# Optimization experiments

Hardware: AMD Instinct MI355X
Metric: run time of the kernel (lower is better)

## Reference

```python
import jax, jax.numpy as jnp
import numpy as np

B, L, DK, DV, H, DKL, DVL, R = 64, 4096, 128, 128, 4, 64, 128, 128


def setup_inputs() -> dict:
    key = jax.random.key(0)
    ks = jax.random.split(key, 7)
    K = jax.random.normal(ks[0], (B, L, DK), dtype=jnp.float32)
    V = jax.random.normal(ks[1], (B, L, DV), dtype=jnp.float32)
    mask = jax.random.uniform(ks[2], (B, L)) < 0.25
    mask = mask.at[:, 0].set(False)
    # Learned parameters (Wq is zeros at init in the original; use small random
    # values so the softmax is non-degenerate for correctness testing)
    Wq = jax.random.normal(ks[3], (H, DKL), dtype=jnp.float32) * 0.02
    Wk = jax.random.normal(ks[4], (DK, H, DKL), dtype=jnp.float32) / np.sqrt(DK)
    Wv = jax.random.normal(ks[5], (DV, H, DVL), dtype=jnp.float32) / np.sqrt(DV)
    Wo = jax.random.normal(ks[6], (H, DVL, R), dtype=jnp.float32) / np.sqrt(H * DVL)
    return {"K": K, "V": V, "mask": mask, "Wq": Wq, "Wk": Wk, "Wv": Wv, "Wo": Wo}


def reference(K, V, mask, Wq, Wk, Wv, Wo):
    # scale = 1/sqrt(dim_q), dim_q == dim_k
    scale = 1.0 / jnp.sqrt(jnp.asarray(K.shape[-1], K.dtype))
    Kp = jnp.einsum('bld,dhk->blhk', K, Wk)          # (B, L, H, DKL)
    Vp = jnp.einsum('ble,ehv->blhv', V, Wv)          # (B, L, H, DVL)
    QK = jnp.einsum('hk,blhk->blh', Wq, Kp)          # (B, L, H)
    QK = jnp.where(mask[..., None], -jnp.inf, QK)    # mask over set axis L
    w = jax.nn.softmax(scale * QK, axis=-2)          # softmax over L (dim=-2)
    # nanmean over the set axis (masked positions contribute w=0; NaN entries,
    # if present in V, are skipped exactly as torch.nanmean does)
    QKV = jnp.nanmean(w[..., None] * Vp, axis=-3)    # (B, H, DVL)
    return jnp.einsum('bhv,hvr->br', QKV, Wo)        # (B, R)
```

## Files before the change

kernel.cpp:

```cpp
#include <hip/hip_runtime.h>
#include <math.h>

#define BB   64
#define LL   4096
#define DKC  128
#define DVC  128
#define HC   4
#define DKLC 64
#define DVLC 128
#define RC   128

#define NCA  64
#define CA   64
#define NCB  16
#define CB   256
#define SUB  4

typedef float f4v __attribute__((ext_vector_type(4)));
__device__ __forceinline__ float4 ntload4(const float4* p) {
    f4v v = __builtin_nontemporal_load((const f4v*)p);
    return make_float4(v.x, v.y, v.z, v.w);
}

__global__ __launch_bounds__(512) void k_foldq(const float* __restrict__ Wq,
                                               const float* __restrict__ Wk,
                                               float* __restrict__ q) {
    int t = threadIdx.x;
    int h = t >> 7;
    int d = t & 127;
    float acc = 0.f;
#pragma unroll 8
    for (int k = 0; k < DKLC; ++k)
        acc += Wq[h * DKLC + k] * Wk[(d * HC + h) * DKLC + k];
    q[h * DKC + d] = acc;
}

__global__ __launch_bounds__(256) void k_score(const float* __restrict__ K,
                                               const int*   __restrict__ mask,
                                               const float* __restrict__ q,
                                               float* __restrict__ P4,
                                               float* __restrict__ stats) {
    const int bid = blockIdx.x;
    const int b   = bid >> 6;
    const int sp  = bid & (NCA - 1);
    const int l0  = sp * CA;
    const int t   = threadIdx.x;
    const int rg  = t >> 5;
    const int i4  = t & 31;

    __shared__ float4 part[CA][33];
    __shared__ float  redm[4][HC];
    __shared__ float  redz[4][HC];

    float4 qf[HC];
#pragma unroll
    for (int h = 0; h < HC; ++h)
        qf[h] = ((const float4*)q)[h * 32 + i4];

    const float4* Kg = (const float4*)(K + ((long)b * LL + l0) * DKC);

#pragma unroll
    for (int it = 0; it < CA / 8; ++it) {
        int r = it * 8 + rg;
        float4 kv = ntload4(&Kg[r * 32 + i4]);
        float4 d;
        d.x = kv.x*qf[0].x + kv.y*qf[0].y + kv.z*qf[0].z + kv.w*qf[0].w;
        d.y = kv.x*qf[1].x + kv.y*qf[1].y + kv.z*qf[1].z + kv.w*qf[1].w;
        d.z = kv.x*qf[2].x + kv.y*qf[2].y + kv.z*qf[2].z + kv.w*qf[2].w;
        d.w = kv.x*qf[3].x + kv.y*qf[3].y + kv.z*qf[3].z + kv.w*qf[3].w;
        part[r][i4] = d;
    }
    __syncthreads();

    const int r2 = t >> 2;
    const int h2 = t & 3;
    float s = 0.f;
#pragma unroll
    for (int c = 0; c < 32; ++c)
        s += ((const float*)part)[(r2 * 33 + c) * 4 + h2];

    int mk = __builtin_nontemporal_load(mask + (long)b * LL + l0 + r2);
    const float scale = 0.08838834764831844f;
    s = mk ? -INFINITY : s * scale;

    float m = s;
#pragma unroll
    for (int off = 4; off <= 32; off <<= 1)
        m = fmaxf(m, __shfl_xor(m, off));
    if ((t & 63) < 4) redm[t >> 6][h2] = m;
    __syncthreads();
    float mm = fmaxf(fmaxf(redm[0][h2], redm[1][h2]),
                     fmaxf(redm[2][h2], redm[3][h2]));
    float mu = (mm == -INFINITY) ? 0.f : mm;

    float p = expf(s - mu);
    float z = p;
#pragma unroll
    for (int off = 4; off <= 32; off <<= 1)
        z += __shfl_xor(z, off);
    if ((t & 63) < 4) redz[t >> 6][h2] = z;
    if (t < HC) stats[(long)bid * 8 + t] = mm;
    __syncthreads();
    if (t < HC)
        stats[(long)bid * 8 + 4 + t] =
            redz[0][t] + redz[1][t] + redz[2][t] + redz[3][t];

    P4[((long)b * LL + l0) * 4 + t] = p;
}

__global__ __launch_bounds__(256) void k_wv(const float* __restrict__ V,
                                            const float* __restrict__ P4,
                                            const float* __restrict__ stats,
                                            float* __restrict__ partWV) {
    const int bid = blockIdx.x;
    const int b   = bid >> 4;
    const int spB = bid & (NCB - 1);
    const int l0  = spB * CB;
    const int t   = threadIdx.x;
    const int rg  = t >> 5;
    const int i4  = t & 31;
    const int w   = t >> 6;

    __shared__ float4 red[4][32][HC];

    float ma[SUB][HC];
#pragma unroll
    for (int j = 0; j < SUB; ++j)
#pragma unroll
        for (int h = 0; h < HC; ++h)
            ma[j][h] = stats[((long)b * NCA + spB * SUB + j) * 8 + h];
    float4 f4[SUB];
#pragma unroll
    for (int h = 0; h < HC; ++h) {
        float m4 = fmaxf(fmaxf(ma[0][h], ma[1][h]), fmaxf(ma[2][h], ma[3][h]));
        float mu4 = (m4 == -INFINITY) ? 0.f : m4;
#pragma unroll
        for (int j = 0; j < SUB; ++j) {
            float f = (ma[j][h] == -INFINITY) ? 0.f : expf(ma[j][h] - mu4);
            ((float*)&f4[j])[h] = f;
        }
    }

    float4 acc[HC];
#pragma unroll
    for (int h = 0; h < HC; ++h) acc[h] = make_float4(0.f, 0.f, 0.f, 0.f);

    const float4* Vb = (const float4*)(V + ((long)b * LL + l0) * DVC);
    const float4* Pb = (const float4*)P4 + (long)b * LL + l0;

#pragma unroll
    for (int j = 0; j < SUB; ++j) {
        float4 fj = f4[j];
#pragma unroll 8
        for (int it = 0; it < 8; ++it) {
            int r = j * 64 + it * 8 + rg;
            float4 w4 = Pb[r];
            float4 vv = ntload4(&Vb[r * 32 + i4]);
            float w0 = w4.x * fj.x, w1 = w4.y * fj.y;
            float w2 = w4.z * fj.z, w3 = w4.w * fj.w;
            acc[0].x += w0*vv.x; acc[0].y += w0*vv.y; acc[0].z += w0*vv.z; acc[0].w += w0*vv.w;
            acc[1].x += w1*vv.x; acc[1].y += w1*vv.y; acc[1].z += w1*vv.z; acc[1].w += w1*vv.w;
            acc[2].x += w2*vv.x; acc[2].y += w2*vv.y; acc[2].z += w2*vv.z; acc[2].w += w2*vv.w;
            acc[3].x += w3*vv.x; acc[3].y += w3*vv.y; acc[3].z += w3*vv.z; acc[3].w += w3*vv.w;
        }
    }

#pragma unroll
    for (int h = 0; h < HC; ++h) {
        acc[h].x += __shfl_xor(acc[h].x, 32);
        acc[h].y += __shfl_xor(acc[h].y, 32);
        acc[h].z += __shfl_xor(acc[h].z, 32);
        acc[h].w += __shfl_xor(acc[h].w, 32);
    }
    if ((t & 63) < 32) {
#pragma unroll
        for (int h = 0; h < HC; ++h) red[w][i4][h] = acc[h];
    }
    __syncthreads();
    if (t < 128) {
        int h = t >> 5, c = t & 31;
        float4 s0 = red[0][c][h], s1 = red[1][c][h];
        float4 s2 = red[2][c][h], s3 = red[3][c][h];
        float4 o;
        o.x = s0.x + s1.x + s2.x + s3.x;
        o.y = s0.y + s1.y + s2.y + s3.y;
        o.z = s0.z + s1.z + s2.z + s3.z;
        o.w = s0.w + s1.w + s2.w + s3.w;
        ((float4*)partWV)[((long)bid * HC + h) * (DVC / 4) + c] = o;
    }
}

__global__ __launch_bounds__(256) void k_out(const float* __restrict__ stats,
                                             const float* __restrict__ partWV,
                                             const float* __restrict__ Wv,
                                             const float* __restrict__ Wo,
                                             float* __restrict__ out) {
    int b = blockIdx.x;
    int t = threadIdx.x;
    __shared__ float WV[HC][DVC];
    __shared__ float QKV[HC * DVLC];
    __shared__ float sc[NCB][HC];
    __shared__ float zinv[HC];

    {
        int h2 = t >> 6, a = t & 63;
        float ma = stats[((long)b * NCA + a) * 8 + h2];
        float za = stats[((long)b * NCA + a) * 8 + 4 + h2];
        float m = ma;
#pragma unroll
        for (int off = 32; off; off >>= 1) m = fmaxf(m, __shfl_xor(m, off));
        float f  = (ma == -INFINITY) ? 0.f : expf(ma - m);
        float fz = f * za;
#pragma unroll
        for (int off = 32; off; off >>= 1) fz += __shfl_xor(fz, off);
        float m4 = ma;
        m4 = fmaxf(m4, __shfl_xor(m4, 1));
        m4 = fmaxf(m4, __shfl_xor(m4, 2));
        if ((a & 3) == 0) sc[a >> 2][h2] = (m4 == -INFINITY) ? 0.f : expf(m4 - m);
        if (a == 0) zinv[h2] = 1.0f / fz;
    }
    __syncthreads();

    for (int j = t; j < HC * DVC; j += 256) {
        int h = j >> 7, e = j & 127;
        float a = 0.f;
#pragma unroll 8
        for (int p = 0; p < NCB; ++p)
            a += sc[p][h] * partWV[(((long)b * NCB + p) * HC + h) * DVC + e];
        WV[h][e] = a * zinv[h];
    }
    __syncthreads();

    for (int j = t; j < HC * DVLC; j += 256) {
        int h = j >> 7, vv = j & 127;
        float a = 0.f;
#pragma unroll 8
        for (int e = 0; e < DVC; ++e)
            a += WV[h][e] * Wv[(e * HC + h) * DVLC + vv];
        QKV[j] = a * (1.0f / LL);
    }
    __syncthreads();

    for (int r = t; r < RC; r += 256) {
        float a = 0.f;
#pragma unroll 8
        for (int i = 0; i < HC * DVLC; ++i)
            a += QKV[i] * Wo[i * RC + r];
        out[b * RC + r] = a;
    }
}

extern "C" void kernel_launch(void* const* d_in, const int* in_sizes, int n_in,
                              void* d_out, int out_size, void* d_ws, size_t ws_size,
                              hipStream_t stream) {
    (void)in_sizes; (void)n_in; (void)out_size; (void)ws_size;
    const float* K    = (const float*)d_in[0];
    const float* V    = (const float*)d_in[1];
    const int*   mask = (const int*)  d_in[2];
    const float* Wq   = (const float*)d_in[3];
    const float* Wk   = (const float*)d_in[4];
    const float* Wv   = (const float*)d_in[5];
    const float* Wo   = (const float*)d_in[6];
    float* out = (float*)d_out;

    float* q      = (float*)d_ws;
    float* stats  = q + 512;
    float* partWV = stats + (long)BB * NCA * 8;
    float* P4     = partWV + (long)BB * NCB * HC * DVC;

    k_foldq<<<1, 512, 0, stream>>>(Wq, Wk, q);
    k_score<<<BB * NCA, 256, 0, stream>>>(K, mask, q, P4, stats);
    k_wv<<<BB * NCB, 256, 0, stream>>>(V, P4, stats, partWV);
    k_out<<<BB, 256, 0, stream>>>(stats, partWV, Wv, Wo, out);
}
```

Measured before the change: 79.89 us.

## Fuse score and weighted-V passes into one kernel per 64-row chunk

Merges the score/softmax-stat kernel and the weighted-V accumulation kernel into a single kernel, so each 64-row chunk computes its probabilities into shared memory and immediately uses them against V. This drops the global P4 round trip and one kernel launch. It also restructures the K dot product so each thread handles two float4s. In exchange, partWV becomes four times larger (64 chunks instead of 16), which enlarges the partial-sum reduction in the output kernel. Shared memory is reused for the final reduction.

```diff
diff --git a/kernel.cpp b/kernel.cpp
--- a/kernel.cpp
+++ b/kernel.cpp
@@ -12,9 +12,6 @@
 
 #define NCA  64
 #define CA   64
-#define NCB  16
-#define CB   256
-#define SUB  4
 
 typedef float f4v __attribute__((ext_vector_type(4)));
 __device__ __forceinline__ float4 ntload4(const float4* p) {
@@ -35,136 +32,106 @@
     q[h * DKC + d] = acc;
 }
 
-__global__ __launch_bounds__(256) void k_score(const float* __restrict__ K,
+__global__ __launch_bounds__(256) void k_fused(const float* __restrict__ K,
+                                               const float* __restrict__ V,
                                                const int*   __restrict__ mask,
                                                const float* __restrict__ q,
-                                               float* __restrict__ P4,
-                                               float* __restrict__ stats) {
+                                               float* __restrict__ stats,
+                                               float* __restrict__ partWV) {
     const int bid = blockIdx.x;
     const int b   = bid >> 6;
-    const int sp  = bid & (NCA - 1);
-    const int l0  = sp * CA;
+    const int a   = bid & (NCA - 1);
+    const int l0  = a * CA;
     const int t   = threadIdx.x;
-    const int rg  = t >> 5;
-    const int i4  = t & 31;
-
-    __shared__ float4 part[CA][33];
+
+    __shared__ float4 partS[CA][17];
+    __shared__ float  P4s[CA * HC];
     __shared__ float  redm[4][HC];
     __shared__ float  redz[4][HC];
 
-    float4 qf[HC];
-#pragma unroll
-    for (int h = 0; h < HC; ++h)
-        qf[h] = ((const float4*)q)[h * 32 + i4];
-
-    const float4* Kg = (const float4*)(K + ((long)b * LL + l0) * DKC);
-
-#pragma unroll
-    for (int it = 0; it < CA / 8; ++it) {
-        int r = it * 8 + rg;
-        float4 kv = ntload4(&Kg[r * 32 + i4]);
-        float4 d;
-        d.x = kv.x*qf[0].x + kv.y*qf[0].y + kv.z*qf[0].z + kv.w*qf[0].w;
-        d.y = kv.x*qf[1].x + kv.y*qf[1].y + kv.z*qf[1].z + kv.w*qf[1].w;
-        d.z = kv.x*qf[2].x + kv.y*qf[2].y + kv.z*qf[2].z + kv.w*qf[2].w;
-        d.w = kv.x*qf[3].x + kv.y*qf[3].y + kv.z*qf[3].z + kv.w*qf[3].w;
-        part[r][i4] = d;
-    }
-    __syncthreads();
-
-    const int r2 = t >> 2;
-    const int h2 = t & 3;
-    float s = 0.f;
-#pragma unroll
-    for (int c = 0; c < 32; ++c)
-        s += ((const float*)part)[(r2 * 33 + c) * 4 + h2];
-
-    int mk = __builtin_nontemporal_load(mask + (long)b * LL + l0 + r2);
-    const float scale = 0.08838834764831844f;
-    s = mk ? -INFINITY : s * scale;
-
-    float m = s;
-#pragma unroll
-    for (int off = 4; off <= 32; off <<= 1)
-        m = fmaxf(m, __shfl_xor(m, off));
-    if ((t & 63) < 4) redm[t >> 6][h2] = m;
-    __syncthreads();
-    float mm = fmaxf(fmaxf(redm[0][h2], redm[1][h2]),
-                     fmaxf(redm[2][h2], redm[3][h2]));
-    float mu = (mm == -INFINITY) ? 0.f : mm;
-
-    float p = expf(s - mu);
-    float z = p;
-#pragma unroll
-    for (int off = 4; off <= 32; off <<= 1)
-        z += __shfl_xor(z, off);
-    if ((t & 63) < 4) redz[t >> 6][h2] = z;
-    if (t < HC) stats[(long)bid * 8 + t] = mm;
-    __syncthreads();
-    if (t < HC)
-        stats[(long)bid * 8 + 4 + t] =
-            redz[0][t] + redz[1][t] + redz[2][t] + redz[3][t];
-
-    P4[((long)b * LL + l0) * 4 + t] = p;
-}
-
-__global__ __launch_bounds__(256) void k_wv(const float* __restrict__ V,
-                                            const float* __restrict__ P4,
-                                            const float* __restrict__ stats,
-                                            float* __restrict__ partWV) {
-    const int bid = blockIdx.x;
-    const int b   = bid >> 4;
-    const int spB = bid & (NCB - 1);
-    const int l0  = spB * CB;
-    const int t   = threadIdx.x;
-    const int rg  = t >> 5;
+    {
+        const int rg = t >> 4;
+        const int i8 = t & 15;
+        float4 qf1[HC], qf2[HC];
+#pragma unroll
+        for (int h = 0; h < HC; ++h) {
+            qf1[h] = ((const float4*)q)[h * 32 + i8];
+            qf2[h] = ((const float4*)q)[h * 32 + i8 + 16];
+        }
+        const float4* Kg = (const float4*)(K + ((long)b * LL + l0) * DKC);
+#pragma unroll
+        for (int it = 0; it < CA / 16; ++it) {
+            int r = it * 16 + rg;
+            float4 k1 = ntload4(&Kg[r * 32 + i8]);
+            float4 k2 = ntload4(&Kg[r * 32 + i8 + 16]);
+            float4 d;
+            d.x = k1.x*qf1[0].x + k1.y*qf1[0].y + k1.z*qf1[0].z + k1.w*qf1[0].w
+                + k2.x*qf2[0].x + k2.y*qf2[0].y + k2.z*qf2[0].z + k2.w*qf2[0].w;
+            d.y = k1.x*qf1[1].x + k1.y*qf1[1].y + k1.z*qf1[1].z + k1.w*qf1[1].w
+                + k2.x*qf2[1].x + k2.y*qf2[1].y + k2.z*qf2[1].z + k2.w*qf2[1].w;
+            d.z = k1.x*qf1[2].x + k1.y*qf1[2].y + k1.z*qf1[2].z + k1.w*qf1[2].w
+                + k2.x*qf2[2].x + k2.y*qf2[2].y + k2.z*qf2[2].z + k2.w*qf2[2].w;
+            d.w = k1.x*qf1[3].x + k1.y*qf1[3].y + k1.z*qf1[3].z + k1.w*qf1[3].w
+                + k2.x*qf2[3].x + k2.y*qf2[3].y + k2.z*qf2[3].z + k2.w*qf2[3].w;
+            partS[r][i8] = d;
+        }
+    }
+    __syncthreads();
+
+    {
+        const int r2 = t >> 2;
+        const int h2 = t & 3;
+        float s = 0.f;
+#pragma unroll
+        for (int c = 0; c < 16; ++c)
+            s += ((const float*)partS)[(r2 * 17 + c) * 4 + h2];
+
+        int mk = __builtin_nontemporal_load(mask + (long)b * LL + l0 + r2);
+        const float scale = 0.08838834764831844f;
+        s = mk ? -INFINITY : s * scale;
+
+        float m = s;
+#pragma unroll
+        for (int off = 4; off <= 32; off <<= 1)
+            m = fmaxf(m, __shfl_xor(m, off));
+        if ((t & 63) < 4) redm[t >> 6][h2] = m;
+        __syncthreads();
+        float mm = fmaxf(fmaxf(redm[0][h2], redm[1][h2]),
+                         fmaxf(redm[2][h2], redm[3][h2]));
+        float mu = (mm == -INFINITY) ? 0.f : mm;
+
+        float p = expf(s - mu);
+        float z = p;
+#pragma unroll
+        for (int off = 4; off <= 32; off <<= 1)
+            z += __shfl_xor(z, off);
+        if ((t & 63) < 4) redz[t >> 6][h2] = z;
+        P4s[t] = p;
+        if (t < HC) stats[(long)bid * 8 + t] = mm;
+        __syncthreads();
+        if (t < HC)
+            stats[(long)bid * 8 + 4 + t] =
+                redz[0][t] + redz[1][t] + redz[2][t] + redz[3][t];
+    }
+
+    const int rg3 = t >> 5;
     const int i4  = t & 31;
     const int w   = t >> 6;
-
-    __shared__ float4 red[4][32][HC];
-
-    float ma[SUB][HC];
-#pragma unroll
-    for (int j = 0; j < SUB; ++j)
-#pragma unroll
-        for (int h = 0; h < HC; ++h)
-            ma[j][h] = stats[((long)b * NCA + spB * SUB + j) * 8 + h];
-    float4 f4[SUB];
-#pragma unroll
-    for (int h = 0; h < HC; ++h) {
-        float m4 = fmaxf(fmaxf(ma[0][h], ma[1][h]), fmaxf(ma[2][h], ma[3][h]));
-        float mu4 = (m4 == -INFINITY) ? 0.f : m4;
-#pragma unroll
-        for (int j = 0; j < SUB; ++j) {
-            float f = (ma[j][h] == -INFINITY) ? 0.f : expf(ma[j][h] - mu4);
-            ((float*)&f4[j])[h] = f;
-        }
-    }
-
     float4 acc[HC];
 #pragma unroll
     for (int h = 0; h < HC; ++h) acc[h] = make_float4(0.f, 0.f, 0.f, 0.f);
 
     const float4* Vb = (const float4*)(V + ((long)b * LL + l0) * DVC);
-    const float4* Pb = (const float4*)P4 + (long)b * LL + l0;
-
-#pragma unroll
-    for (int j = 0; j < SUB; ++j) {
-        float4 fj = f4[j];
-#pragma unroll 8
-        for (int it = 0; it < 8; ++it) {
-            int r = j * 64 + it * 8 + rg;
-            float4 w4 = Pb[r];
-            float4 vv = ntload4(&Vb[r * 32 + i4]);
-            float w0 = w4.x * fj.x, w1 = w4.y * fj.y;
-            float w2 = w4.z * fj.z, w3 = w4.w * fj.w;
-            acc[0].x += w0*vv.x; acc[0].y += w0*vv.y; acc[0].z += w0*vv.z; acc[0].w += w0*vv.w;
-            acc[1].x += w1*vv.x; acc[1].y += w1*vv.y; acc[1].z += w1*vv.z; acc[1].w += w1*vv.w;
-            acc[2].x += w2*vv.x; acc[2].y += w2*vv.y; acc[2].z += w2*vv.z; acc[2].w += w2*vv.w;
-            acc[3].x += w3*vv.x; acc[3].y += w3*vv.y; acc[3].z += w3*vv.z; acc[3].w += w3*vv.w;
-        }
-    }
-
+#pragma unroll
+    for (int it = 0; it < CA / 8; ++it) {
+        int r = it * 8 + rg3;
+        float4 vv = ntload4(&Vb[r * 32 + i4]);
+        float4 w4 = ((const float4*)P4s)[r];
+        acc[0].x += w4.x*vv.x; acc[0].y += w4.x*vv.y; acc[0].z += w4.x*vv.z; acc[0].w += w4.x*vv.w;
+        acc[1].x += w4.y*vv.x; acc[1].y += w4.y*vv.y; acc[1].z += w4.y*vv.z; acc[1].w += w4.y*vv.w;
+        acc[2].x += w4.z*vv.x; acc[2].y += w4.z*vv.y; acc[2].z += w4.z*vv.z; acc[2].w += w4.z*vv.w;
+        acc[3].x += w4.w*vv.x; acc[3].y += w4.w*vv.y; acc[3].z += w4.w*vv.z; acc[3].w += w4.w*vv.w;
+    }
 #pragma unroll
     for (int h = 0; h < HC; ++h) {
         acc[h].x += __shfl_xor(acc[h].x, 32);
@@ -172,6 +139,8 @@
         acc[h].z += __shfl_xor(acc[h].z, 32);
         acc[h].w += __shfl_xor(acc[h].w, 32);
     }
+    float4 (*red)[32][HC] = (float4 (*)[32][HC])partS;
+    __syncthreads();
     if ((t & 63) < 32) {
 #pragma unroll
         for (int h = 0; h < HC; ++h) red[w][i4][h] = acc[h];
@@ -199,7 +168,7 @@
     int t = threadIdx.x;
     __shared__ float WV[HC][DVC];
     __shared__ float QKV[HC * DVLC];
-    __shared__ float sc[NCB][HC];
+    __shared__ float sc[NCA][HC];
     __shared__ float zinv[HC];
 
     {
@@ -210,43 +179,40 @@
 #pragma unroll
         for (int off = 32; off; off >>= 1) m = fmaxf(m, __shfl_xor(m, off));
         float f  = (ma == -INFINITY) ? 0.f : expf(ma - m);
+        sc[a][h2] = f;
         float fz = f * za;
 #pragma unroll
         for (int off = 32; off; off >>= 1) fz += __shfl_xor(fz, off);
-        float m4 = ma;
-        m4 = fmaxf(m4, __shfl_xor(m4, 1));
-        m4 = fmaxf(m4, __shfl_xor(m4, 2));
-        if ((a & 3) == 0) sc[a >> 2][h2] = (m4 == -INFINITY) ? 0.f : expf(m4 - m);
         if (a == 0) zinv[h2] = 1.0f / fz;
     }
     __syncthreads();
 
     for (int j = t; j < HC * DVC; j += 256) {
         int h = j >> 7, e = j & 127;
-        float a = 0.f;
-#pragma unroll 8
-        for (int p = 0; p < NCB; ++p)
-            a += sc[p][h] * partWV[(((long)b * NCB + p) * HC + h) * DVC + e];
-        WV[h][e] = a * zinv[h];
+        float acc = 0.f;
+#pragma unroll 8
+        for (int p = 0; p < NCA; ++p)
+            acc += sc[p][h] * partWV[(((long)b * NCA + p) * HC + h) * DVC + e];
+        WV[h][e] = acc * zinv[h];
     }
     __syncthreads();
 
     for (int j = t; j < HC * DVLC; j += 256) {
         int h = j >> 7, vv = j & 127;
-        float a = 0.f;
+        float acc = 0.f;
 #pragma unroll 8
         for (int e = 0; e < DVC; ++e)
-            a += WV[h][e] * Wv[(e * HC + h) * DVLC + vv];
-        QKV[j] = a * (1.0f / LL);
+            acc += WV[h][e] * Wv[(e * HC + h) * DVLC + vv];
+        QKV[j] = acc * (1.0f / LL);
     }
     __syncthreads();
 
     for (int r = t; r < RC; r += 256) {
-        float a = 0.f;
+        float acc = 0.f;
 #pragma unroll 8
         for (int i = 0; i < HC * DVLC; ++i)
-            a += QKV[i] * Wo[i * RC + r];
-        out[b * RC + r] = a;
+            acc += QKV[i] * Wo[i * RC + r];
+        out[b * RC + r] = acc;
     }
 }
 
@@ -266,10 +232,8 @@
     float* q      = (float*)d_ws;
     float* stats  = q + 512;
     float* partWV = stats + (long)BB * NCA * 8;
-    float* P4     = partWV + (long)BB * NCB * HC * DVC;
 
     k_foldq<<<1, 512, 0, stream>>>(Wq, Wk, q);
-    k_score<<<BB * NCA, 256, 0, stream>>>(K, mask, q, P4, stats);
-    k_wv<<<BB * NCB, 256, 0, stream>>>(V, P4, stats, partWV);
+    k_fused<<<BB * NCA, 256, 0, stream>>>(K, V, mask, q, stats, partWV);
     k_out<<<BB, 256, 0, stream>>>(stats, partWV, Wv, Wo, out);
 }
```

After: 77.86 us. 1.03x faster.
